# Kernel tuning notes

Measured on AMD Instinct MI355X. Metric: run time of the kernel, lower is better.

Reference implementation:

```python
import jax, jax.numpy as jnp
import numpy as np

RESHAPE = 640
NC = 80
TOPK = 10
EPS = 1e-7      # module eps (BCEloss / log clamps)
IOU_EPS = 1e-9  # iou() eps
DIS = 2.5
BS = 16
NUM_GT = 32


def make_anchors():
    pts, strides = [], []
    for s in (8, 16, 32):
        n = RESHAPE // s
        ys, xs = jnp.meshgrid(jnp.arange(n, dtype=jnp.float32),
                              jnp.arange(n, dtype=jnp.float32), indexing='ij')
        pts.append(jnp.stack([xs.ravel(), ys.ravel()], -1))
        strides.append(jnp.full((n * n, 1), float(s), dtype=jnp.float32))
    return jnp.concatenate(pts, 0), jnp.concatenate(strides, 0)


def setup_inputs() -> dict:
    key = jax.random.key(0)
    ks = jax.random.split(key, 8)
    anchor_points, stride_tensor = make_anchors()
    hw = anchor_points.shape[0]

    def rand_boxes(k, lead):
        k1, k2 = jax.random.split(k)
        c = jax.random.uniform(k1, lead + (2,), minval=80.0, maxval=560.0)
        wh = jax.random.uniform(k2, lead + (2,), minval=20.0, maxval=160.0)
        return jnp.concatenate([c - wh / 2, c + wh / 2], -1)

    pred_boxes = rand_boxes(ks[0], (BS, hw))
    gt_boxes = rand_boxes(ks[1], (BS, NUM_GT))
    counts = jax.random.randint(ks[2], (BS,), 8, NUM_GT + 1)
    mask_gt = jnp.arange(NUM_GT)[None, :] < counts[:, None]
    pred_scores = jax.random.uniform(ks[3], (BS, hw, NC)) * 0.98 + 0.01
    pred_conf = jax.random.uniform(ks[4], (BS, hw, 1)) * 0.98 + 0.01
    gt_labels = jax.random.randint(ks[5], (BS, NUM_GT, 1), 0, NC)
    return dict(pred_boxes=pred_boxes, gt_boxes=gt_boxes, mask_gt=mask_gt,
                pred_scores=pred_scores, pred_conf=pred_conf, gt_labels=gt_labels,
                anchor_points=anchor_points, stride_tensor=stride_tensor)


def box_iou(p, g, ciou=False, eps=IOU_EPS):
    # p, g broadcastable [..., 4] in xyxy; matches the torch iou() exactly
    b1x1, b1y1, b1x2, b1y2 = p[..., 0], p[..., 1], p[..., 2], p[..., 3]
    b2x1, b2y1, b2x2, b2y2 = g[..., 0], g[..., 1], g[..., 2], g[..., 3]
    w1, h1 = b1x2 - b1x1, b1y2 - b1y1 + eps
    w2, h2 = b2x2 - b2x1, b2y2 - b2y1 + eps
    inter = (jnp.maximum(jnp.minimum(b1x2, b2x2) - jnp.maximum(b1x1, b2x1), 0.0)
             * jnp.maximum(jnp.minimum(b1y2, b2y2) - jnp.maximum(b1y1, b2y1), 0.0))
    union = w1 * h1 + w2 * h2 - inter + eps
    iou = inter / union
    if ciou:
        cw = jnp.maximum(b1x2, b2x2) - jnp.minimum(b1x1, b2x1)
        ch = jnp.maximum(b1y2, b2y2) - jnp.minimum(b1y1, b2y1)
        c2 = cw ** 2 + ch ** 2 + eps
        d2 = ((b2x1 + b2x2 - b1x1 - b1x2) ** 2 + (b2y1 + b2y2 - b1y1 - b1y2) ** 2) / 4
        v = (4.0 / np.pi ** 2) * (jnp.arctan(w2 / h2) - jnp.arctan(w1 / h1)) ** 2
        alpha = jax.lax.stop_gradient(v / (v - iou + (1.0 + eps)))
        return iou - (d2 / c2 + v * alpha)
    return iou


def _forward(pred_boxes, gt_boxes, mask_gt, pred_scores, pred_conf, gt_labels,
             anchor_points, stride_tensor):
    bs, hw, nc = pred_scores.shape
    G = mask_gt.shape[1]
    dt = pred_boxes.dtype

    apd = (anchor_points + 0.5) * stride_tensor          # (hw, 2)
    gb = gt_boxes[:, :, None, :]                          # (bs, G, 1, 4)
    # strict in-box test
    lt = apd[None, None] - gb[..., :2]
    rb = gb[..., 2:] - apd[None, None]
    in_boxes = (lt > 0).all(-1) & (rb > 0).all(-1)        # (bs, G, hw)
    # center prior (radius 2.5 * stride)
    ctr = (gb[..., :2] + gb[..., 2:]) / 2
    dis = DIS * stride_tensor                             # (hw, 1) -> broadcast (hw, 2)
    lt2 = apd[None, None] - (ctr - dis)
    rb2 = (ctr + dis) - apd[None, None]
    in_centers = (lt2 > 0).all(-1) & (rb2 > 0).all(-1)
    fg = in_boxes | in_centers
    in_both = in_boxes & in_centers

    iou_val = box_iou(pred_boxes[:, None], gt_boxes[:, :, None])   # (bs, G, hw)
    iou_cost = -jnp.log(iou_val + EPS)

    # torch F.binary_cross_entropy with one-hot target zeroed outside fg:
    # sum_c BCE = S + fg * (nll0[label] - nll1[label]), logs clamped at -100
    nll1 = -jnp.maximum(jnp.log(1.0 - pred_scores), -100.0)        # (bs, hw, nc)
    S = nll1.sum(-1)                                               # (bs, hw)
    bidx = jnp.arange(bs)[:, None, None]
    aidx = jnp.arange(hw)[None, None, :]
    lab = gt_labels[..., 0][:, :, None]
    pl = pred_scores[bidx, aidx, lab]                              # (bs, G, hw)
    nll0_l = -jnp.maximum(jnp.log(pl), -100.0)
    nll1_l = -jnp.maximum(jnp.log(1.0 - pl), -100.0)
    cls_cost = S[:, None] + fg.astype(dt) * (nll0_l - nll1_l)

    cost = cls_cost + 3.0 * iou_cost + 100000.0 * (~in_both).astype(dt)
    cost = jnp.where(mask_gt[:, :, None], cost, jnp.asarray(1e6, dt))

    # dynamic-k: sum of top-min(TOPK, num_fg) ious, floor, clamp(min=1)
    top_iou = jax.lax.top_k(jnp.where(fg, iou_val, -jnp.inf), TOPK)[0]
    pt_num = jnp.maximum(jnp.where(jnp.isfinite(top_iou), top_iou, 0.0).sum(-1),
                         1.0).astype(jnp.int32)
    pt_num = jnp.where(mask_gt, pt_num, 0)                         # invalid gt -> 0

    # pick pt_num smallest-cost anchors per gt via ranks (emulates topk(largest=False))
    ranks = jnp.argsort(jnp.argsort(cost, axis=-1), axis=-1)
    pt_mask = ranks < pt_num[..., None]                            # (bs, G, hw) bool

    # resolve anchors claimed by >1 gt: keep only min-cost gt
    count = pt_mask.sum(1)                                         # (bs, hw)
    best = jnp.argmin(cost, axis=1)                                # (bs, hw)
    onehot = best[:, None, :] == jnp.arange(G)[None, :, None]
    pt_mask = jnp.where(count[:, None] > 1, onehot, pt_mask)

    m = pt_mask.astype(dt)
    num_pts = m.sum((1, 2))                                        # (bs,)

    ciou_v = box_iou(pred_boxes[:, None], gt_boxes[:, :, None], ciou=True)
    l0 = (((1.0 - ciou_v) * m).sum((1, 2)) / num_pts).sum()

    # module BCEloss (with EPS) vs one-hot target, summed over classes
    Se = (-jnp.log(1.0 - pred_scores + EPS)).sum(-1)               # (bs, hw)
    bce = Se[:, None] + (-jnp.log(pl + EPS)) - (-jnp.log(1.0 - pl + EPS))
    l1 = ((bce * m).sum((1, 2)) / num_pts).sum()

    gt_conf = (pt_mask.sum(1) > 0).astype(dt)                      # (bs, hw)
    pc = pred_conf[..., 0]
    bce_c = -gt_conf * jnp.log(pc + EPS) - (1.0 - gt_conf) * jnp.log(1.0 - pc + EPS)
    l2 = (bce_c.sum(-1) / num_pts).sum()
    return l0, l1, l2


def reference(pred_boxes, gt_boxes, mask_gt, pred_scores, pred_conf, gt_labels,
              anchor_points, stride_tensor):
    return _forward(pred_boxes, gt_boxes, mask_gt, pred_scores, pred_conf,
                    gt_labels, anchor_points, stride_tensor)
```

## Files before the change

kernel.cpp:

```cpp
#include <hip/hip_runtime.h>
#include <math.h>

#define TPB 256
#define KTOP 10
#define GMAX 32
#define NITER 33

__device__ __forceinline__ bool read_maskgt(const void* p, int i) {
    const unsigned char* b = (const unsigned char*)p;
    if (b[1] != 0) return b[i] != 0;
    return ((const int*)p)[i] != 0;
}

__global__ void k0_init(float* out, int* numpts, int bs) {
    int t = threadIdx.x;
    if (t < 3) out[t] = 0.0f;
    if (t < bs) numpts[t] = 0;
}

__global__ void k1_scores(const float* __restrict__ ps, float* __restrict__ S,
                          float* __restrict__ Se, int rows, int NC) {
    int r = blockIdx.x * 4 + (threadIdx.x >> 6);
    int lane = threadIdx.x & 63;
    if (r >= rows) return;
    const float* row = ps + (long)r * NC;
    float s = 0.f, se = 0.f;
    for (int c = lane; c < NC; c += 64) {
        float p = row[c];
        s  += -fmaxf(logf(1.0f - p), -100.0f);
        se += -logf(1.0f - p + 1e-7f);
    }
    for (int off = 32; off; off >>= 1) {
        s  += __shfl_down(s, off);
        se += __shfl_down(se, off);
    }
    if (lane == 0) { S[r] = s; Se[r] = se; }
}

__global__ void k2a_cost(const float* __restrict__ pred_boxes,
                         const float* __restrict__ gt_boxes,
                         const void*  mask_gt,
                         const float* __restrict__ ps,
                         const int*   __restrict__ labels,
                         const float* __restrict__ anchors,
                         const float* __restrict__ strides,
                         const float* __restrict__ S,
                         float* __restrict__ cost,
                         unsigned char* __restrict__ mask,
                         unsigned char* __restrict__ best,
                         int G, int HW, int NC) {
    __shared__ float4 s_gb[GMAX];
    __shared__ float  s_ctrx[GMAX], s_ctry[GMAX];
    __shared__ int    s_lab[GMAX];
    __shared__ int    s_val[GMAX];

    int b = blockIdx.y;
    int tid = threadIdx.x;
    if (tid < G) {
        int pr = b * G + tid;
        float4 gb = ((const float4*)gt_boxes)[pr];
        s_gb[tid] = gb;
        s_ctrx[tid] = (gb.x + gb.z) * 0.5f;
        s_ctry[tid] = (gb.y + gb.w) * 0.5f;
        s_lab[tid] = labels[pr];
        s_val[tid] = read_maskgt(mask_gt, pr) ? 1 : 0;
    }
    __syncthreads();

    int a = blockIdx.x * TPB + tid;
    if (a >= HW) return;

    const float4 pb = ((const float4*)(pred_boxes + (long)b * HW * 4))[a];
    float ax = anchors[2 * a], ay = anchors[2 * a + 1];
    float st = strides[a];
    float apx = (ax + 0.5f) * st, apy = (ay + 0.5f) * st;
    float dis = 2.5f * st;
    float Sa = S[(long)b * HW + a];
    float w1 = pb.z - pb.x, h1 = pb.w - pb.y + 1e-9f;
    float w1h1 = w1 * h1;
    const float* __restrict__ row = ps + ((long)b * HW + a) * NC;

    float bestc = 3.4e38f;
    int bestg = 0;

#pragma unroll
    for (int g = 0; g < GMAX; ++g) {
        if (g >= G) break;
        long oidx = ((long)(b * G + g)) * HW + a;
        float c;
        if (!s_val[g]) {
            c = 1e6f;
        } else {
            float pl = row[s_lab[g]];
            float4 gb = s_gb[g];
            float gx1 = gb.x, gy1 = gb.y, gx2 = gb.z, gy2 = gb.w;
            bool in_boxes = (apx - gx1 > 0.f) & (apy - gy1 > 0.f) &
                            (gx2 - apx > 0.f) & (gy2 - apy > 0.f);
            float ctrx = s_ctrx[g], ctry = s_ctry[g];
            bool in_centers = (apx - (ctrx - dis) > 0.f) & (apy - (ctry - dis) > 0.f) &
                              ((ctrx + dis) - apx > 0.f) & ((ctry + dis) - apy > 0.f);
            bool fg = in_boxes | in_centers;
            bool in_both = in_boxes & in_centers;

            float w2 = gx2 - gx1, h2 = gy2 - gy1 + 1e-9f;
            float iw = fminf(pb.z, gx2) - fmaxf(pb.x, gx1);
            float ih = fminf(pb.w, gy2) - fmaxf(pb.y, gy1);
            float inter = fmaxf(iw, 0.f) * fmaxf(ih, 0.f);
            float uni = w1h1 + w2 * h2 - inter + 1e-9f;
            float iou = inter / uni;
            float iou_cost = -logf(iou + 1e-7f);

            float nll0 = -fmaxf(logf(pl), -100.f);
            float nll1 = -fmaxf(logf(1.f - pl), -100.f);
            float cls = Sa + (fg ? (nll0 - nll1) : 0.f);
            c = cls + 3.f * iou_cost + (in_both ? 0.f : 100000.f);
        }
        cost[oidx] = c;
        mask[oidx] = 0;
        if (c < bestc) { bestc = c; bestg = g; }
    }
    best[(long)b * HW + a] = (unsigned char)bestg;
}

__device__ __forceinline__ void radix_sel(const unsigned* keys, int kth,
                                          unsigned* s_hist, int* s_bin, int* s_cum,
                                          int tid, unsigned& outKey, int& outCnt) {
    unsigned pref = 0;
    int kk = kth, cnt = 0;
#pragma unroll
    for (int lvl = 0; lvl < 4; ++lvl) {
        const int sh = 24 - 8 * lvl;
        s_hist[tid] = 0u;
        __syncthreads();
        int curBin = -1; unsigned curCnt = 0u;
#pragma unroll
        for (int j = 0; j < NITER; ++j) {
            unsigned key = keys[j];
            bool par = (lvl == 0) || ((key >> (sh + 8)) == pref);
            if (par) {
                int d = (int)((key >> sh) & 255u);
                if (d == curBin) curCnt++;
                else {
                    if (curBin >= 0) atomicAdd(&s_hist[curBin], curCnt);
                    curBin = d; curCnt = 1u;
                }
            }
        }
        if (curBin >= 0) atomicAdd(&s_hist[curBin], curCnt);
        __syncthreads();
        if (tid < 64) {
            unsigned h0 = s_hist[4 * tid + 0], h1 = s_hist[4 * tid + 1];
            unsigned h2 = s_hist[4 * tid + 2], h3 = s_hist[4 * tid + 3];
            int tot = (int)(h0 + h1 + h2 + h3);
            int incl = tot;
            for (int off = 1; off < 64; off <<= 1) {
                int o = __shfl_up(incl, off);
                if (tid >= off) incl += o;
            }
            int ex = incl - tot;
            bool hit = (ex < kk) && (incl >= kk);
            unsigned long long bal = __ballot(hit);
            int src = __ffsll((unsigned long long)bal) - 1;
            if (tid == src) {
                int c = ex; int bsel = 4 * tid;
                if (c + (int)h0 < kk) { c += (int)h0; bsel++;
                    if (c + (int)h1 < kk) { c += (int)h1; bsel++;
                        if (c + (int)h2 < kk) { c += (int)h2; bsel++; } } }
                *s_bin = bsel; *s_cum = c;
            }
        }
        __syncthreads();
        int bin = *s_bin, c = *s_cum;
        kk -= c; cnt += c;
        pref = (pref << 8) | (unsigned)bin;
        __syncthreads();
    }
    outKey = pref; outCnt = cnt;
}

__global__ void k2_sel(const float* __restrict__ pred_boxes,
                       const float* __restrict__ gt_boxes,
                       const void*  mask_gt,
                       const float* __restrict__ anchors,
                       const float* __restrict__ strides,
                       const float* __restrict__ cost,
                       unsigned char* __restrict__ mask,
                       int G, int HW) {
    __shared__ unsigned s_hist[256];
    __shared__ int s_bin, s_cum;
    __shared__ float s_red[256];
    __shared__ int s_ptn;
    __shared__ unsigned s_tie[256];
    __shared__ int s_tiecnt;

    int pair = blockIdx.x;
    if (!read_maskgt(mask_gt, pair)) return;
    int b = pair / G;
    int tid = threadIdx.x;

    const float4 gb = ((const float4*)gt_boxes)[pair];
    const float gx1 = gb.x, gy1 = gb.y, gx2 = gb.z, gy2 = gb.w;
    const float ctrx = (gx1 + gx2) * 0.5f, ctry = (gy1 + gy2) * 0.5f;
    const float w2 = gx2 - gx1, h2 = gy2 - gy1 + 1e-9f;

    const float* pbb  = pred_boxes + (long)b * HW * 4;
    const float* crow = cost + (long)pair * HW;

    unsigned ck[NITER], ik[NITER];
#pragma unroll
    for (int j = 0; j < NITER; ++j) {
        int a = j * TPB + tid;
        unsigned ckey = 0xFFFFFFFFu, ikey = 0xFFFFFFFFu;
        if (a < HW) {
            float4 pb = ((const float4*)pbb)[a];
            float ax = anchors[2 * a], ay = anchors[2 * a + 1];
            float st = strides[a];
            float apx = (ax + 0.5f) * st, apy = (ay + 0.5f) * st;
            bool in_boxes = (apx - gx1 > 0.f) & (apy - gy1 > 0.f) &
                            (gx2 - apx > 0.f) & (gy2 - apy > 0.f);
            float dis = 2.5f * st;
            bool in_centers = (apx - (ctrx - dis) > 0.f) & (apy - (ctry - dis) > 0.f) &
                              ((ctrx + dis) - apx > 0.f) & ((ctry + dis) - apy > 0.f);
            bool fg = in_boxes | in_centers;

            float w1 = pb.z - pb.x, h1 = pb.w - pb.y + 1e-9f;
            float iw = fminf(pb.z, gx2) - fmaxf(pb.x, gx1);
            float ih = fminf(pb.w, gy2) - fmaxf(pb.y, gy1);
            float inter = fmaxf(iw, 0.f) * fmaxf(ih, 0.f);
            float uni = w1 * h1 + w2 * h2 - inter + 1e-9f;
            float iou = inter / uni;

            float c = crow[a];
            unsigned cb = __float_as_uint(c);
            ckey = cb ^ (((int)cb < 0) ? 0xFFFFFFFFu : 0x80000000u);
            ikey = fg ? ~__float_as_uint(iou) : 0xFFFFFFFFu;
        }
        ck[j] = ckey; ik[j] = ikey;
    }

    unsigned K10; int cnt10;
    radix_sel(ik, KTOP, s_hist, &s_bin, &s_cum, tid, K10, cnt10);

    float ls = 0.f;
#pragma unroll
    for (int j = 0; j < NITER; ++j)
        if (ik[j] < K10) ls += __uint_as_float(~ik[j]);
    s_red[tid] = ls;
    __syncthreads();
    for (int s = 128; s; s >>= 1) {
        if (tid < s) s_red[tid] += s_red[tid + s];
        __syncthreads();
    }
    if (tid == 0) {
        float tot = s_red[0] + (float)(KTOP - cnt10) * __uint_as_float(~K10);
        s_ptn = (int)fmaxf(tot, 1.0f);
    }
    __syncthreads();
    int ptn = s_ptn;

    unsigned Kc; int cntc;
    radix_sel(ck, ptn, s_hist, &s_bin, &s_cum, tid, Kc, cntc);
    int tneed = ptn - cntc;

    if (tid == 0) s_tiecnt = 0;
    __syncthreads();
    unsigned char* mrow = mask + (long)pair * HW;
#pragma unroll
    for (int j = 0; j < NITER; ++j) {
        int a = j * TPB + tid;
        if (a < HW) {
            if (ck[j] < Kc) mrow[a] = 1;
            else if (ck[j] == Kc) {
                int p = atomicAdd(&s_tiecnt, 1);
                if (p < 256) s_tie[p] = (unsigned)a;
            }
        }
    }
    __syncthreads();
    int m = min(s_tiecnt, 256);
    if (tneed >= m) {
        for (int e = tid; e < m; e += TPB) mrow[s_tie[e]] = 1;
    } else if (tneed > 0) {
        for (int e = tid; e < m; e += TPB) {
            unsigned my = s_tie[e];
            int r = 0;
            for (int q = 0; q < m; ++q) r += (s_tie[q] < my) ? 1 : 0;
            if (r < tneed) mrow[my] = 1;
        }
    }
}

__global__ void k3_assign(const unsigned char* __restrict__ best,
                          unsigned char* __restrict__ mask,
                          unsigned char* __restrict__ gtconf,
                          int* __restrict__ numpts,
                          int G, int HW) {
    __shared__ int red[TPB];
    int b = blockIdx.y;
    int a = blockIdx.x * TPB + threadIdx.x;
    int cntf = 0;
    if (a < HW) {
        int cnt = 0;
        for (int g = 0; g < G; ++g)
            cnt += mask[((long)(b * G + g)) * HW + a];
        if (cnt > 1) {
            unsigned int bits = 1u << best[(long)b * HW + a];
            for (int g = 0; g < G; ++g)
                mask[((long)(b * G + g)) * HW + a] = (unsigned char)((bits >> g) & 1u);
        }
        cntf = (cnt > 1) ? 1 : cnt;
        gtconf[(long)b * HW + a] = (unsigned char)(cntf > 0 ? 1 : 0);
    }
    red[threadIdx.x] = cntf;
    __syncthreads();
    for (int s = TPB / 2; s; s >>= 1) {
        if (threadIdx.x < s) red[threadIdx.x] += red[threadIdx.x + s];
        __syncthreads();
    }
    if (threadIdx.x == 0 && red[0] > 0) atomicAdd(&numpts[b], red[0]);
}

__global__ void k4_pair(const float* __restrict__ pred_boxes,
                        const float* __restrict__ gt_boxes,
                        const float* __restrict__ ps,
                        const int*   __restrict__ labels,
                        const float* __restrict__ Se,
                        const unsigned char* __restrict__ mask,
                        const int* __restrict__ numpts,
                        float* __restrict__ out,
                        int G, int HW, int NC) {
    __shared__ float r0[TPB];
    __shared__ float r1[TPB];
    int tid = threadIdx.x;
    int pair = blockIdx.x;
    int b = pair / G;
    const unsigned char* mrow = mask + (long)pair * HW;
    const float4 gb = ((const float4*)gt_boxes)[pair];
    float gx1 = gb.x, gy1 = gb.y, gx2 = gb.z, gy2 = gb.w;
    float w2 = gx2 - gx1, h2 = gy2 - gy1 + 1e-9f;
    int lab = labels[pair];
    const float* pbb   = pred_boxes + (long)b * HW * 4;
    const float* psb   = ps + (long)b * HW * NC;
    const float* Serow = Se + (long)b * HW;
    float at2 = atanf(w2 / h2);
    float s0 = 0.f, s1 = 0.f;
    for (int a = tid; a < HW; a += TPB) {
        if (!mrow[a]) continue;
        float4 pb = ((const float4*)pbb)[a];
        float w1 = pb.z - pb.x, h1 = pb.w - pb.y + 1e-9f;
        float iw = fminf(pb.z, gx2) - fmaxf(pb.x, gx1);
        float ih = fminf(pb.w, gy2) - fmaxf(pb.y, gy1);
        float inter = fmaxf(iw, 0.f) * fmaxf(ih, 0.f);
        float uni = w1 * h1 + w2 * h2 - inter + 1e-9f;
        float iou = inter / uni;
        float cw = fmaxf(pb.z, gx2) - fminf(pb.x, gx1);
        float ch = fmaxf(pb.w, gy2) - fminf(pb.y, gy1);
        float c2 = cw * cw + ch * ch + 1e-9f;
        float dx = gx1 + gx2 - pb.x - pb.z;
        float dy = gy1 + gy2 - pb.y - pb.w;
        float d2 = (dx * dx + dy * dy) * 0.25f;
        float dat = at2 - atanf(w1 / h1);
        float v = 0.4052847345693511f * dat * dat;
        float alpha = v / (v - iou + 1.0f);
        float ciou = iou - (d2 / c2 + v * alpha);
        s0 += 1.0f - ciou;
        float pl = psb[(long)a * NC + lab];
        s1 += Serow[a] - logf(pl + 1e-7f) + logf(1.f - pl + 1e-7f);
    }
    r0[tid] = s0; r1[tid] = s1;
    __syncthreads();
    for (int s = TPB / 2; s; s >>= 1) {
        if (tid < s) { r0[tid] += r0[tid + s]; r1[tid] += r1[tid + s]; }
        __syncthreads();
    }
    if (tid == 0 && (r0[0] != 0.f || r1[0] != 0.f)) {
        float np = (float)numpts[b];
        atomicAdd(out + 0, r0[0] / np);
        atomicAdd(out + 1, r1[0] / np);
    }
}

__global__ void k4_conf(const float* __restrict__ pred_conf,
                        const unsigned char* __restrict__ gtconf,
                        const int* __restrict__ numpts,
                        float* __restrict__ out, int HW) {
    __shared__ float red[TPB];
    int b = blockIdx.y;
    int a = blockIdx.x * TPB + threadIdx.x;
    float v = 0.f;
    if (a < HW) {
        float pc = pred_conf[(long)b * HW + a];
        v = gtconf[(long)b * HW + a] ? -logf(pc + 1e-7f) : -logf(1.f - pc + 1e-7f);
    }
    red[threadIdx.x] = v;
    __syncthreads();
    for (int s = TPB / 2; s; s >>= 1) {
        if (threadIdx.x < s) red[threadIdx.x] += red[threadIdx.x + s];
        __syncthreads();
    }
    if (threadIdx.x == 0) atomicAdd(out + 2, red[0] / (float)numpts[b]);
}

extern "C" void kernel_launch(void* const* d_in, const int* in_sizes, int n_in,
                              void* d_out, int out_size, void* d_ws, size_t ws_size,
                              hipStream_t stream) {
    const float* pred_boxes = (const float*)d_in[0];
    const float* gt_boxes   = (const float*)d_in[1];
    const void*  mask_gt    = d_in[2];
    const float* ps         = (const float*)d_in[3];
    const float* pred_conf  = (const float*)d_in[4];
    const int*   gt_labels  = (const int*)d_in[5];
    const float* anchors    = (const float*)d_in[6];
    const float* strides    = (const float*)d_in[7];
    float* out = (float*)d_out;

    const int HW = in_sizes[7];
    const int BS = in_sizes[4] / HW;
    const int G  = in_sizes[5] / BS;
    const int NC = in_sizes[3] / (BS * HW);

    char* w = (char*)d_ws;
    float* S  = (float*)w;                    w += (size_t)BS * HW * 4;
    float* Se = (float*)w;                    w += (size_t)BS * HW * 4;
    float* cost = (float*)w;                  w += (size_t)BS * G * HW * 4;
    int* numpts = (int*)w;                    w += 256;
    unsigned char* mask   = (unsigned char*)w; w += (size_t)BS * G * HW;
    unsigned char* gtconf = (unsigned char*)w; w += (size_t)BS * HW;
    unsigned char* best   = (unsigned char*)w;

    k0_init<<<1, 64, 0, stream>>>(out, numpts, BS);

    int rows = BS * HW;
    k1_scores<<<(rows + 3) / 4, TPB, 0, stream>>>(ps, S, Se, rows, NC);

    dim3 g2a((HW + TPB - 1) / TPB, BS);
    k2a_cost<<<g2a, TPB, 0, stream>>>(pred_boxes, gt_boxes, mask_gt, ps, gt_labels,
                                      anchors, strides, S, cost, mask, best, G, HW, NC);

    k2_sel<<<BS * G, TPB, 0, stream>>>(pred_boxes, gt_boxes, mask_gt, anchors,
                                       strides, cost, mask, G, HW);

    dim3 g3((HW + TPB - 1) / TPB, BS);
    k3_assign<<<g3, TPB, 0, stream>>>(best, mask, gtconf, numpts, G, HW);

    k4_pair<<<BS * G, TPB, 0, stream>>>(pred_boxes, gt_boxes, ps, gt_labels, Se,
                                        mask, numpts, out, G, HW, NC);

    k4_conf<<<g3, TPB, 0, stream>>>(pred_conf, gtconf, numpts, out, HW);
}
```

Baseline: 214.1 us.

## Fuse score row sums into cost kernel and conf BCE into assign kernel

Removes the separate per-row score-sum kernel: the cost kernel now reads each anchor's 80-class row with float4 loads and computes both log-sum terms itself. This avoids the S buffer and one launch. The confidence BCE is folded into the assign kernel as a per-batch atomic sum, and the pair kernel adds it to the output, removing the gtconf buffer and the final launch. The trade-off is that the row sums now run one anchor per thread with strided float4 loads (320-byte stride between adjacent threads), which coalesces worse than the earlier wave-per-row reduction and adds register pressure to the cost kernel.

```diff
diff --git a/kernel.cpp b/kernel.cpp
--- a/kernel.cpp
+++ b/kernel.cpp
@@ -12,29 +12,10 @@
     return ((const int*)p)[i] != 0;
 }
 
-__global__ void k0_init(float* out, int* numpts, int bs) {
+__global__ void k0_init(float* out, int* numpts, float* bce_sum, int bs) {
     int t = threadIdx.x;
     if (t < 3) out[t] = 0.0f;
-    if (t < bs) numpts[t] = 0;
-}
-
-__global__ void k1_scores(const float* __restrict__ ps, float* __restrict__ S,
-                          float* __restrict__ Se, int rows, int NC) {
-    int r = blockIdx.x * 4 + (threadIdx.x >> 6);
-    int lane = threadIdx.x & 63;
-    if (r >= rows) return;
-    const float* row = ps + (long)r * NC;
-    float s = 0.f, se = 0.f;
-    for (int c = lane; c < NC; c += 64) {
-        float p = row[c];
-        s  += -fmaxf(logf(1.0f - p), -100.0f);
-        se += -logf(1.0f - p + 1e-7f);
-    }
-    for (int off = 32; off; off >>= 1) {
-        s  += __shfl_down(s, off);
-        se += __shfl_down(se, off);
-    }
-    if (lane == 0) { S[r] = s; Se[r] = se; }
+    if (t < bs) { numpts[t] = 0; bce_sum[t] = 0.0f; }
 }
 
 __global__ void k2a_cost(const float* __restrict__ pred_boxes,
@@ -44,7 +25,7 @@
                          const int*   __restrict__ labels,
                          const float* __restrict__ anchors,
                          const float* __restrict__ strides,
-                         const float* __restrict__ S,
+                         float* __restrict__ Se,
                          float* __restrict__ cost,
                          unsigned char* __restrict__ mask,
                          unsigned char* __restrict__ best,
@@ -70,15 +51,30 @@
     int a = blockIdx.x * TPB + tid;
     if (a >= HW) return;
 
+    const float* __restrict__ row = ps + ((long)b * HW + a) * NC;
+    float Sa = 0.f, se = 0.f;
+    int c = 0;
+    for (; c + 4 <= NC; c += 4) {
+        float4 v = *(const float4*)(row + c);
+        Sa += -fmaxf(logf(1.0f - v.x), -100.0f) - fmaxf(logf(1.0f - v.y), -100.0f)
+            - fmaxf(logf(1.0f - v.z), -100.0f) - fmaxf(logf(1.0f - v.w), -100.0f);
+        se += -logf(1.0f - v.x + 1e-7f) - logf(1.0f - v.y + 1e-7f)
+            - logf(1.0f - v.z + 1e-7f) - logf(1.0f - v.w + 1e-7f);
+    }
+    for (; c < NC; ++c) {
+        float p = row[c];
+        Sa += -fmaxf(logf(1.0f - p), -100.0f);
+        se += -logf(1.0f - p + 1e-7f);
+    }
+    Se[(long)b * HW + a] = se;
+
     const float4 pb = ((const float4*)(pred_boxes + (long)b * HW * 4))[a];
     float ax = anchors[2 * a], ay = anchors[2 * a + 1];
     float st = strides[a];
     float apx = (ax + 0.5f) * st, apy = (ay + 0.5f) * st;
     float dis = 2.5f * st;
-    float Sa = S[(long)b * HW + a];
     float w1 = pb.z - pb.x, h1 = pb.w - pb.y + 1e-9f;
     float w1h1 = w1 * h1;
-    const float* __restrict__ row = ps + ((long)b * HW + a) * NC;
 
     float bestc = 3.4e38f;
     int bestg = 0;
@@ -87,9 +83,9 @@
     for (int g = 0; g < GMAX; ++g) {
         if (g >= G) break;
         long oidx = ((long)(b * G + g)) * HW + a;
-        float c;
+        float cst;
         if (!s_val[g]) {
-            c = 1e6f;
+            cst = 1e6f;
         } else {
             float pl = row[s_lab[g]];
             float4 gb = s_gb[g];
@@ -113,11 +109,11 @@
             float nll0 = -fmaxf(logf(pl), -100.f);
             float nll1 = -fmaxf(logf(1.f - pl), -100.f);
             float cls = Sa + (fg ? (nll0 - nll1) : 0.f);
-            c = cls + 3.f * iou_cost + (in_both ? 0.f : 100000.f);
-        }
-        cost[oidx] = c;
+            cst = cls + 3.f * iou_cost + (in_both ? 0.f : 100000.f);
+        }
+        cost[oidx] = cst;
         mask[oidx] = 0;
-        if (c < bestc) { bestc = c; bestg = g; }
+        if (cst < bestc) { bestc = cst; bestg = g; }
     }
     best[(long)b * HW + a] = (unsigned char)bestg;
 }
@@ -291,14 +287,17 @@
 }
 
 __global__ void k3_assign(const unsigned char* __restrict__ best,
+                          const float* __restrict__ pred_conf,
                           unsigned char* __restrict__ mask,
-                          unsigned char* __restrict__ gtconf,
                           int* __restrict__ numpts,
+                          float* __restrict__ bce_sum,
                           int G, int HW) {
-    __shared__ int red[TPB];
+    __shared__ int   red[TPB];
+    __shared__ float redf[TPB];
     int b = blockIdx.y;
     int a = blockIdx.x * TPB + threadIdx.x;
     int cntf = 0;
+    float vbce = 0.f;
     if (a < HW) {
         int cnt = 0;
         for (int g = 0; g < G; ++g)
@@ -309,15 +308,23 @@
                 mask[((long)(b * G + g)) * HW + a] = (unsigned char)((bits >> g) & 1u);
         }
         cntf = (cnt > 1) ? 1 : cnt;
-        gtconf[(long)b * HW + a] = (unsigned char)(cntf > 0 ? 1 : 0);
+        float pc = pred_conf[(long)b * HW + a];
+        vbce = (cntf > 0) ? -logf(pc + 1e-7f) : -logf(1.f - pc + 1e-7f);
     }
     red[threadIdx.x] = cntf;
+    redf[threadIdx.x] = vbce;
     __syncthreads();
     for (int s = TPB / 2; s; s >>= 1) {
-        if (threadIdx.x < s) red[threadIdx.x] += red[threadIdx.x + s];
-        __syncthreads();
-    }
-    if (threadIdx.x == 0 && red[0] > 0) atomicAdd(&numpts[b], red[0]);
+        if (threadIdx.x < s) {
+            red[threadIdx.x]  += red[threadIdx.x + s];
+            redf[threadIdx.x] += redf[threadIdx.x + s];
+        }
+        __syncthreads();
+    }
+    if (threadIdx.x == 0) {
+        if (red[0] > 0) atomicAdd(&numpts[b], red[0]);
+        atomicAdd(&bce_sum[b], redf[0]);
+    }
 }
 
 __global__ void k4_pair(const float* __restrict__ pred_boxes,
@@ -327,6 +334,7 @@
                         const float* __restrict__ Se,
                         const unsigned char* __restrict__ mask,
                         const int* __restrict__ numpts,
+                        const float* __restrict__ bce_sum,
                         float* __restrict__ out,
                         int G, int HW, int NC) {
     __shared__ float r0[TPB];
@@ -373,32 +381,15 @@
         if (tid < s) { r0[tid] += r0[tid + s]; r1[tid] += r1[tid + s]; }
         __syncthreads();
     }
-    if (tid == 0 && (r0[0] != 0.f || r1[0] != 0.f)) {
+    if (tid == 0) {
         float np = (float)numpts[b];
-        atomicAdd(out + 0, r0[0] / np);
-        atomicAdd(out + 1, r1[0] / np);
-    }
-}
-
-__global__ void k4_conf(const float* __restrict__ pred_conf,
-                        const unsigned char* __restrict__ gtconf,
-                        const int* __restrict__ numpts,
-                        float* __restrict__ out, int HW) {
-    __shared__ float red[TPB];
-    int b = blockIdx.y;
-    int a = blockIdx.x * TPB + threadIdx.x;
-    float v = 0.f;
-    if (a < HW) {
-        float pc = pred_conf[(long)b * HW + a];
-        v = gtconf[(long)b * HW + a] ? -logf(pc + 1e-7f) : -logf(1.f - pc + 1e-7f);
-    }
-    red[threadIdx.x] = v;
-    __syncthreads();
-    for (int s = TPB / 2; s; s >>= 1) {
-        if (threadIdx.x < s) red[threadIdx.x] += red[threadIdx.x + s];
-        __syncthreads();
-    }
-    if (threadIdx.x == 0) atomicAdd(out + 2, red[0] / (float)numpts[b]);
+        if (r0[0] != 0.f || r1[0] != 0.f) {
+            atomicAdd(out + 0, r0[0] / np);
+            atomicAdd(out + 1, r1[0] / np);
+        }
+        if ((pair % G) == 0)
+            atomicAdd(out + 2, bce_sum[b] / np);
+    }
 }
 
 extern "C" void kernel_launch(void* const* d_in, const int* in_sizes, int n_in,
@@ -420,31 +411,25 @@
     const int NC = in_sizes[3] / (BS * HW);
 
     char* w = (char*)d_ws;
-    float* S  = (float*)w;                    w += (size_t)BS * HW * 4;
     float* Se = (float*)w;                    w += (size_t)BS * HW * 4;
     float* cost = (float*)w;                  w += (size_t)BS * G * HW * 4;
     int* numpts = (int*)w;                    w += 256;
-    unsigned char* mask   = (unsigned char*)w; w += (size_t)BS * G * HW;
-    unsigned char* gtconf = (unsigned char*)w; w += (size_t)BS * HW;
-    unsigned char* best   = (unsigned char*)w;
-
-    k0_init<<<1, 64, 0, stream>>>(out, numpts, BS);
-
-    int rows = BS * HW;
-    k1_scores<<<(rows + 3) / 4, TPB, 0, stream>>>(ps, S, Se, rows, NC);
+    float* bce_sum = (float*)w;               w += 256;
+    unsigned char* mask = (unsigned char*)w;  w += (size_t)BS * G * HW;
+    unsigned char* best = (unsigned char*)w;
+
+    k0_init<<<1, 64, 0, stream>>>(out, numpts, bce_sum, BS);
 
     dim3 g2a((HW + TPB - 1) / TPB, BS);
     k2a_cost<<<g2a, TPB, 0, stream>>>(pred_boxes, gt_boxes, mask_gt, ps, gt_labels,
-                                      anchors, strides, S, cost, mask, best, G, HW, NC);
+                                      anchors, strides, Se, cost, mask, best, G, HW, NC);
 
     k2_sel<<<BS * G, TPB, 0, stream>>>(pred_boxes, gt_boxes, mask_gt, anchors,
                                        strides, cost, mask, G, HW);
 
     dim3 g3((HW + TPB - 1) / TPB, BS);
-    k3_assign<<<g3, TPB, 0, stream>>>(best, mask, gtconf, numpts, G, HW);
+    k3_assign<<<g3, TPB, 0, stream>>>(best, pred_conf, mask, numpts, bce_sum, G, HW);
 
     k4_pair<<<BS * G, TPB, 0, stream>>>(pred_boxes, gt_boxes, ps, gt_labels, Se,
-                                        mask, numpts, out, G, HW, NC);
-
-    k4_conf<<<g3, TPB, 0, stream>>>(pred_conf, gtconf, numpts, out, HW);
-}
+                                        mask, numpts, bce_sum, out, G, HW, NC);
+}
```

Result: faster. 200.8 us (-6.2%).
